# Kernel optimization log

Measured on AMD Instinct MI355X. Metric: run time of the kernel, lower is better.

The kernel has to match this reference:

```python
import jax, jax.numpy as jnp
import numpy as np

N_EMBD = 768
N_HEAD = 12
B, T = 2, 2048


def setup_inputs() -> dict:
    key = jax.random.key(0)
    ks = jax.random.split(key, 8)
    C = N_EMBD
    s = 0.02
    return {
        "x": jax.random.normal(ks[0], (B, T, C), jnp.float32),
        "ln1_g": jnp.ones((C,), jnp.float32),
        "ln1_b": jnp.zeros((C,), jnp.float32),
        "w_attn": jax.random.normal(ks[1], (C, 3 * C), jnp.float32) * s,
        "b_attn": jnp.zeros((3 * C,), jnp.float32),
        "w_attn_proj": jax.random.normal(ks[2], (C, C), jnp.float32) * s,
        "b_attn_proj": jnp.zeros((C,), jnp.float32),
        "ln2_g": jnp.ones((C,), jnp.float32),
        "ln2_b": jnp.zeros((C,), jnp.float32),
        "w_fc": jax.random.normal(ks[3], (C, 4 * C), jnp.float32) * s,
        "b_fc": jnp.zeros((4 * C,), jnp.float32),
        "w_mlp_proj": jax.random.normal(ks[4], (4 * C, C), jnp.float32) * s,
        "b_mlp_proj": jnp.zeros((C,), jnp.float32),
    }


def _layernorm(x, g, b, eps=1e-5):
    mu = jnp.mean(x, axis=-1, keepdims=True)
    var = jnp.mean(jnp.square(x - mu), axis=-1, keepdims=True)
    return (x - mu) * jax.lax.rsqrt(var + eps) * g + b


def _new_gelu(x):
    c = np.sqrt(2.0 / np.pi).astype(np.float32)
    return 0.5 * x * (1.0 + jnp.tanh(c * (x + 0.044715 * x * x * x)))


def _block(x, ln1_g, ln1_b, w_attn, b_attn, w_attn_proj, b_attn_proj,
           ln2_g, ln2_b, w_fc, b_fc, w_mlp_proj, b_mlp_proj):
    Bx, Tx, C = x.shape
    hd = C // N_HEAD
    h = _layernorm(x, ln1_g, ln1_b)
    qkv = h @ w_attn + b_attn  # [B,T,3C]
    q, k, v = jnp.split(qkv, 3, axis=-1)
    # [B,H,T,hd]
    q = q.reshape(Bx, Tx, N_HEAD, hd).transpose(0, 2, 1, 3)
    k = k.reshape(Bx, Tx, N_HEAD, hd).transpose(0, 2, 1, 3)
    v = v.reshape(Bx, Tx, N_HEAD, hd).transpose(0, 2, 1, 3)
    att = jnp.einsum('bhqd,bhkd->bhqk', q, k) * (1.0 / np.sqrt(hd))
    causal = jnp.tril(jnp.ones((Tx, Tx), bool))
    att = jnp.where(causal[None, None], att, -jnp.inf)
    att = jax.nn.softmax(att, axis=-1)
    y = jnp.einsum('bhqk,bhkd->bhqd', att, v)
    y = y.transpose(0, 2, 1, 3).reshape(Bx, Tx, C)
    x = x + y @ w_attn_proj + b_attn_proj
    h2 = _layernorm(x, ln2_g, ln2_b)
    x = x + _new_gelu(h2 @ w_fc + b_fc) @ w_mlp_proj + b_mlp_proj
    return x


def reference(x, ln1_g, ln1_b, w_attn, b_attn, w_attn_proj, b_attn_proj,
              ln2_g, ln2_b, w_fc, b_fc, w_mlp_proj, b_mlp_proj):
    return _block(x, ln1_g, ln1_b, w_attn, b_attn, w_attn_proj, b_attn_proj,
                  ln2_g, ln2_b, w_fc, b_fc, w_mlp_proj, b_mlp_proj)
```

## Files before the change

kernel.cpp:

```cpp
#include <hip/hip_runtime.h>
#include <hip/hip_bf16.h>
#include <math.h>

#define N_EMBD 768
#define N_HEAD 12
#define BATCH  2
#define SEQ    2048
#define ROWS   (BATCH*SEQ)
#define C3     (3*N_EMBD)

typedef __bf16 bf16;
typedef __attribute__((ext_vector_type(8))) __bf16 bf16x8;
typedef __attribute__((ext_vector_type(4))) float f32x4;

__device__ __forceinline__ void async16(const bf16* g, bf16* l) {
    __builtin_amdgcn_global_load_lds(
        (const __attribute__((address_space(1))) uint32_t*)g,
        (__attribute__((address_space(3))) uint32_t*)l, 16, 0, 0);
}

__global__ __launch_bounds__(256) void k_transpose_cast(
    const float* __restrict__ in, bf16* __restrict__ out, int K, int N)
{
    __shared__ bf16 tile[32][33];
    int n0 = blockIdx.x * 32, k0 = blockIdx.y * 32;
    int tc = threadIdx.x & 31, tr = threadIdx.x >> 5;
    #pragma unroll
    for (int i = 0; i < 4; i++) {
        int r = tr + i * 8;
        tile[r][tc] = (bf16)in[(size_t)(k0 + r) * N + n0 + tc];
    }
    __syncthreads();
    #pragma unroll
    for (int i = 0; i < 4; i++) {
        int r = tr + i * 8;
        out[(size_t)(n0 + r) * K + k0 + tc] = tile[tc][r];
    }
}

__global__ __launch_bounds__(256) void k_vtrans(
    const bf16* __restrict__ qkv, bf16* __restrict__ vt)
{
    __shared__ bf16 tile[32][33];
    int tt = blockIdx.x;
    int bh = blockIdx.y;
    int dt = blockIdx.z;
    int b = bh / N_HEAD, h = bh % N_HEAD;
    int tc = threadIdx.x & 31, tr = threadIdx.x >> 5;
    #pragma unroll
    for (int i = 0; i < 4; i++) {
        int r = tr + i * 8;
        tile[r][tc] = qkv[(size_t)(b * SEQ + tt * 32 + r) * C3 + 2 * N_EMBD + h * 64 + dt * 32 + tc];
    }
    __syncthreads();
    #pragma unroll
    for (int i = 0; i < 4; i++) {
        int r = tr + i * 8;
        vt[(size_t)(bh * 64 + dt * 32 + r) * SEQ + tt * 32 + tc] = tile[tc][r];
    }
}

__global__ __launch_bounds__(256) void k_layernorm(
    const float* __restrict__ x, const float* __restrict__ g,
    const float* __restrict__ b, bf16* __restrict__ out)
{
    int wave = threadIdx.x >> 6, lane = threadIdx.x & 63;
    int row = blockIdx.x * 4 + wave;
    const float* xr = x + (size_t)row * N_EMBD;
    float v[12];
    float s = 0.f, sq = 0.f;
    #pragma unroll
    for (int i = 0; i < 12; i++) {
        v[i] = xr[lane + 64 * i];
        s += v[i]; sq += v[i] * v[i];
    }
    #pragma unroll
    for (int off = 32; off > 0; off >>= 1) {
        s  += __shfl_xor(s, off);
        sq += __shfl_xor(sq, off);
    }
    float mu  = s * (1.f / N_EMBD);
    float var = sq * (1.f / N_EMBD) - mu * mu;
    float rs  = rsqrtf(var + 1e-5f);
    bf16* orow = out + (size_t)row * N_EMBD;
    #pragma unroll
    for (int i = 0; i < 12; i++) {
        int c = lane + 64 * i;
        orow[c] = (bf16)((v[i] - mu) * rs * g[c] + b[c]);
    }
}

template<int BN, int ACT, bool RES, bool OUT_BF16>
__global__ __launch_bounds__(256) void k_gemm(
    const bf16* __restrict__ A, const bf16* __restrict__ Bt,
    const float* __restrict__ bias, const float* __restrict__ res,
    void* __restrict__ outp, int M, int N, int K)
{
    constexpr int WC  = BN / 64;
    constexpr int WR  = 4 / WC;
    constexpr int RPW = 128 / WR;
    constexpr int MI  = RPW / 16;
    __shared__ __align__(16) bf16 As[128 * 64];
    __shared__ __align__(16) bf16 Bs[BN * 64];
    int n0 = blockIdx.x * BN, m0 = blockIdx.y * 128;
    int t = threadIdx.x;
    int lane = t & 63, wave = t >> 6;
    int wr = wave / WC, wc = wave % WC;
    int quad = lane >> 4, l16 = lane & 15;

    f32x4 acc[MI][4];
    #pragma unroll
    for (int i = 0; i < MI; i++)
        #pragma unroll
        for (int j = 0; j < 4; j++) acc[i][j] = (f32x4){0.f, 0.f, 0.f, 0.f};

    int sr = t >> 3;
    int sc = t & 7;
    int gsw = (sc ^ (sr & 7)) * 8;

    for (int k0 = 0; k0 < K; k0 += 64) {
        __syncthreads();
        #pragma unroll
        for (int p = 0; p < 4; p++) {
            int r = sr + p * 32;
            async16(&A[(size_t)(m0 + r) * K + k0 + gsw], &As[r * 64 + sc * 8]);
        }
        #pragma unroll
        for (int p = 0; p < BN / 32; p++) {
            int r = sr + p * 32;
            async16(&Bt[(size_t)(n0 + r) * K + k0 + gsw], &Bs[r * 64 + sc * 8]);
        }
        __syncthreads();
        #pragma unroll
        for (int kh = 0; kh < 2; kh++) {
            bf16x8 af[MI], bfv[4];
            #pragma unroll
            for (int i = 0; i < MI; i++)
                af[i]  = *(bf16x8*)&As[(wr * RPW + i * 16 + l16) * 64 + (((quad + 4 * kh) ^ (l16 & 7)) * 8)];
            #pragma unroll
            for (int j = 0; j < 4; j++)
                bfv[j] = *(bf16x8*)&Bs[(wc * 64 + j * 16 + l16) * 64 + (((quad + 4 * kh) ^ (l16 & 7)) * 8)];
            #pragma unroll
            for (int i = 0; i < MI; i++)
                #pragma unroll
                for (int j = 0; j < 4; j++)
                    acc[i][j] = __builtin_amdgcn_mfma_f32_16x16x32_bf16(af[i], bfv[j], acc[i][j], 0, 0, 0);
        }
    }

    float* outf = (float*)outp;
    bf16*  outb = (bf16*)outp;
    #pragma unroll
    for (int i = 0; i < MI; i++) {
        #pragma unroll
        for (int j = 0; j < 4; j++) {
            int col = n0 + wc * 64 + j * 16 + l16;
            float bv = bias[col];
            #pragma unroll
            for (int r = 0; r < 4; r++) {
                int row = m0 + wr * RPW + i * 16 + quad * 4 + r;
                float v = acc[i][j][r] + bv;
                if (ACT == 1) {
                    float z = 0.7978845608f * (v + 0.044715f * v * v * v);
                    v = v / (1.f + __expf(-2.f * z));
                }
                if (RES) v += res[(size_t)row * N + col];
                if (OUT_BF16) outb[(size_t)row * N + col] = (bf16)v;
                else          outf[(size_t)row * N + col] = v;
            }
        }
    }
}

#define PS_S 72
__global__ __launch_bounds__(256) void k_flash(
    const bf16* __restrict__ qkv, const bf16* __restrict__ vt, bf16* __restrict__ y)
{
    __shared__ __align__(16) bf16 Ks[64 * 64];
    __shared__ __align__(16) bf16 VTl[64 * 64];
    __shared__ __align__(16) bf16 Ps[4][16 * PS_S];
    int bid = blockIdx.x;
    int u = bid >> 1, sb = bid & 1;
    int v = u & 31, w = u >> 5;
    int bh = 2 * w + sb;
    int qt = sb ? 31 - v : v;
    int b = bh / N_HEAD, h = bh % N_HEAD;
    int t = threadIdx.x, lane = t & 63, wave = t >> 6;
    int quad = lane >> 4, l16 = lane & 15;
    int qbase = qt * 64 + wave * 16;

    bf16x8 qa[2];
    {
        const bf16* qrow = qkv + (size_t)(b * SEQ + qbase + l16) * C3 + h * 64;
        #pragma unroll
        for (int kh = 0; kh < 2; kh++) {
            union { uint4 u4; bf16 e[8]; bf16x8 vv; } uq;
            uq.u4 = *(const uint4*)&qrow[quad * 8 + kh * 32];
            #pragma unroll
            for (int j = 0; j < 8; j++) uq.e[j] = (bf16)((float)uq.e[j] * 0.125f);
            qa[kh] = uq.vv;
        }
    }
    float l_part[4] = {0.f, 0.f, 0.f, 0.f};
    f32x4 o[4];
    #pragma unroll
    for (int j = 0; j < 4; j++) o[j] = (f32x4){0.f, 0.f, 0.f, 0.f};

    int sr = t >> 3;
    int sc = t & 7;
    int gsw = (sc ^ (sr & 7)) * 8;

    for (int k0 = 0; k0 <= qt * 64; k0 += 64) {
        __syncthreads();
        #pragma unroll
        for (int p = 0; p < 2; p++) {
            int kr = sr + 32 * p;
            async16(&qkv[(size_t)(b * SEQ + k0 + kr) * C3 + N_EMBD + h * 64 + gsw],
                    &Ks[kr * 64 + sc * 8]);
        }
        #pragma unroll
        for (int p = 0; p < 2; p++) {
            int dr = sr + 32 * p;
            async16(&vt[(size_t)(bh * 64 + dr) * SEQ + k0 + gsw],
                    &VTl[dr * 64 + sc * 8]);
        }
        __syncthreads();

        f32x4 s[4];
        #pragma unroll
        for (int nt = 0; nt < 4; nt++) {
            bf16x8 b0 = *(bf16x8*)&Ks[(nt * 16 + l16) * 64 + (((quad    ) ^ (l16 & 7)) * 8)];
            bf16x8 b1 = *(bf16x8*)&Ks[(nt * 16 + l16) * 64 + (((quad + 4) ^ (l16 & 7)) * 8)];
            f32x4 z = (f32x4){0.f, 0.f, 0.f, 0.f};
            z = __builtin_amdgcn_mfma_f32_16x16x32_bf16(qa[0], b0, z, 0, 0, 0);
            z = __builtin_amdgcn_mfma_f32_16x16x32_bf16(qa[1], b1, z, 0, 0, 0);
            s[nt] = z;
        }
        bool diag = (k0 == qt * 64);
        float p[4][4];
        #pragma unroll
        for (int nt = 0; nt < 4; nt++) {
            int key = k0 + nt * 16 + l16;
            #pragma unroll
            for (int r = 0; r < 4; r++) {
                float pv = __expf(s[nt][r]);
                if (diag && key > qbase + quad * 4 + r) pv = 0.f;
                p[nt][r] = pv;
                l_part[r] += pv;
            }
        }
        #pragma unroll
        for (int nt = 0; nt < 4; nt++)
            #pragma unroll
            for (int r = 0; r < 4; r++)
                Ps[wave][(quad * 4 + r) * PS_S + nt * 16 + l16] = (bf16)p[nt][r];
        bf16x8 pa[2];
        #pragma unroll
        for (int kt = 0; kt < 2; kt++)
            pa[kt] = *(bf16x8*)&Ps[wave][l16 * PS_S + kt * 32 + quad * 8];
        #pragma unroll
        for (int jt = 0; jt < 4; jt++) {
            int d = jt * 16 + l16;
            #pragma unroll
            for (int kt = 0; kt < 2; kt++) {
                bf16x8 vb = *(bf16x8*)&VTl[d * 64 + (((quad + 4 * kt) ^ (l16 & 7)) * 8)];
                o[jt] = __builtin_amdgcn_mfma_f32_16x16x32_bf16(pa[kt], vb, o[jt], 0, 0, 0);
            }
        }
    }
    #pragma unroll
    for (int r = 0; r < 4; r++) {
        #pragma unroll
        for (int off = 8; off > 0; off >>= 1) l_part[r] += __shfl_xor(l_part[r], off);
    }
    #pragma unroll
    for (int jt = 0; jt < 4; jt++)
        #pragma unroll
        for (int r = 0; r < 4; r++) {
            int q = qbase + quad * 4 + r;
            y[(size_t)(b * SEQ + q) * N_EMBD + h * 64 + jt * 16 + l16] =
                (bf16)(o[jt][r] / l_part[r]);
        }
}

extern "C" void kernel_launch(void* const* d_in, const int* in_sizes, int n_in,
                              void* d_out, int out_size, void* d_ws, size_t ws_size,
                              hipStream_t stream) {
    const float* x           = (const float*)d_in[0];
    const float* ln1_g       = (const float*)d_in[1];
    const float* ln1_b       = (const float*)d_in[2];
    const float* w_attn      = (const float*)d_in[3];
    const float* b_attn      = (const float*)d_in[4];
    const float* w_attn_proj = (const float*)d_in[5];
    const float* b_attn_proj = (const float*)d_in[6];
    const float* ln2_g       = (const float*)d_in[7];
    const float* ln2_b       = (const float*)d_in[8];
    const float* w_fc        = (const float*)d_in[9];
    const float* b_fc        = (const float*)d_in[10];
    const float* w_mlp_proj  = (const float*)d_in[11];
    const float* b_mlp_proj  = (const float*)d_in[12];

    char* ws = (char*)d_ws;
    size_t off = 0;
    auto alloc = [&](size_t n) -> void* {
        off = (off + 255) & ~(size_t)255;
        void* p = ws + off;
        off += n;
        return p;
    };
    bf16* wqkvT  = (bf16*)alloc((size_t)C3 * N_EMBD * 2);
    bf16* wprojT = (bf16*)alloc((size_t)N_EMBD * N_EMBD * 2);
    bf16* wfcT   = (bf16*)alloc((size_t)4 * N_EMBD * N_EMBD * 2);
    bf16* wmlpT  = (bf16*)alloc((size_t)N_EMBD * 4 * N_EMBD * 2);
    bf16* hbuf   = (bf16*)alloc((size_t)ROWS * N_EMBD * 2);
    float* x2    = (float*)alloc((size_t)ROWS * N_EMBD * 4);
    bf16* yb     = (bf16*)alloc((size_t)ROWS * N_EMBD * 2);
    bf16* vtb    = (bf16*)alloc((size_t)BATCH * N_HEAD * 64 * SEQ * 2);
    bf16* big    = (bf16*)alloc((size_t)ROWS * 4 * N_EMBD * 2);
    bf16* qkvb   = big;
    bf16* actb   = big;

    k_transpose_cast<<<dim3(C3 / 32,     N_EMBD / 32), 256, 0, stream>>>(w_attn,      wqkvT,  N_EMBD, C3);
    k_transpose_cast<<<dim3(N_EMBD / 32, N_EMBD / 32), 256, 0, stream>>>(w_attn_proj, wprojT, N_EMBD, N_EMBD);
    k_transpose_cast<<<dim3(3072 / 32,   N_EMBD / 32), 256, 0, stream>>>(w_fc,        wfcT,   N_EMBD, 3072);
    k_transpose_cast<<<dim3(N_EMBD / 32, 3072 / 32),   256, 0, stream>>>(w_mlp_proj,  wmlpT,  3072,   N_EMBD);

    k_layernorm<<<ROWS / 4, 256, 0, stream>>>(x, ln1_g, ln1_b, hbuf);
    k_gemm<128, 0, false, true ><<<dim3(C3 / 128,  ROWS / 128), 256, 0, stream>>>(hbuf, wqkvT,  b_attn,      nullptr, qkvb, ROWS, C3,     N_EMBD);
    k_vtrans<<<dim3(SEQ / 32, BATCH * N_HEAD, 2), 256, 0, stream>>>(qkvb, vtb);
    k_flash<<<768, 256, 0, stream>>>(qkvb, vtb, yb);
    k_gemm<64,  0, true,  false><<<dim3(N_EMBD / 64, ROWS / 128), 256, 0, stream>>>(yb,   wprojT, b_attn_proj, x,       x2,   ROWS, N_EMBD, N_EMBD);
    k_layernorm<<<ROWS / 4, 256, 0, stream>>>(x2, ln2_g, ln2_b, hbuf);
    k_gemm<128, 1, false, true ><<<dim3(3072 / 128, ROWS / 128), 256, 0, stream>>>(hbuf, wfcT,   b_fc,        nullptr, actb, ROWS, 3072,   N_EMBD);
    k_gemm<64,  0, true,  false><<<dim3(N_EMBD / 64, ROWS / 128), 256, 0, stream>>>(actb, wmlpT,  b_mlp_proj,  x2, (float*)d_out, ROWS, N_EMBD, 3072);
}
```

Before: 297.8 us.

## Fuse V transpose into QKV GEMM, merge weight casts, double-buffer flash loads

```diff
diff --git a/kernel.cpp b/kernel.cpp
--- a/kernel.cpp
+++ b/kernel.cpp
@@ -19,11 +19,21 @@
         (__attribute__((address_space(3))) uint32_t*)l, 16, 0, 0);
 }
 
-__global__ __launch_bounds__(256) void k_transpose_cast(
-    const float* __restrict__ in, bf16* __restrict__ out, int K, int N)
+__global__ __launch_bounds__(256) void k_transpose_all(
+    const float* __restrict__ w0, bf16* __restrict__ o0,
+    const float* __restrict__ w1, bf16* __restrict__ o1,
+    const float* __restrict__ w2, bf16* __restrict__ o2,
+    const float* __restrict__ w3, bf16* __restrict__ o3)
 {
     __shared__ bf16 tile[32][33];
-    int n0 = blockIdx.x * 32, k0 = blockIdx.y * 32;
+    int bid = blockIdx.x;
+    const float* in; bf16* out; int K, N, local;
+    if      (bid < 1728) { in = w0; out = o0; K = 768;  N = 2304; local = bid; }
+    else if (bid < 2304) { in = w1; out = o1; K = 768;  N = 768;  local = bid - 1728; }
+    else if (bid < 4608) { in = w2; out = o2; K = 768;  N = 3072; local = bid - 2304; }
+    else                 { in = w3; out = o3; K = 3072; N = 768;  local = bid - 4608; }
+    int nt = N / 32;
+    int n0 = (local % nt) * 32, k0 = (local / nt) * 32;
     int tc = threadIdx.x & 31, tr = threadIdx.x >> 5;
     #pragma unroll
     for (int i = 0; i < 4; i++) {
@@ -35,28 +45,6 @@
     for (int i = 0; i < 4; i++) {
         int r = tr + i * 8;
         out[(size_t)(n0 + r) * K + k0 + tc] = tile[tc][r];
-    }
-}
-
-__global__ __launch_bounds__(256) void k_vtrans(
-    const bf16* __restrict__ qkv, bf16* __restrict__ vt)
-{
-    __shared__ bf16 tile[32][33];
-    int tt = blockIdx.x;
-    int bh = blockIdx.y;
-    int dt = blockIdx.z;
-    int b = bh / N_HEAD, h = bh % N_HEAD;
-    int tc = threadIdx.x & 31, tr = threadIdx.x >> 5;
-    #pragma unroll
-    for (int i = 0; i < 4; i++) {
-        int r = tr + i * 8;
-        tile[r][tc] = qkv[(size_t)(b * SEQ + tt * 32 + r) * C3 + 2 * N_EMBD + h * 64 + dt * 32 + tc];
-    }
-    __syncthreads();
-    #pragma unroll
-    for (int i = 0; i < 4; i++) {
-        int r = tr + i * 8;
-        vt[(size_t)(bh * 64 + dt * 32 + r) * SEQ + tt * 32 + tc] = tile[tc][r];
     }
 }
 
@@ -90,11 +78,11 @@
     }
 }
 
-template<int BN, int ACT, bool RES, bool OUT_BF16>
+template<int BN, int ACT, bool RES, bool OUT_BF16, bool VOUT>
 __global__ __launch_bounds__(256) void k_gemm(
     const bf16* __restrict__ A, const bf16* __restrict__ Bt,
     const float* __restrict__ bias, const float* __restrict__ res,
-    void* __restrict__ outp, int M, int N, int K)
+    void* __restrict__ outp, bf16* __restrict__ vout, int M, int N, int K)
 {
     constexpr int WC  = BN / 64;
     constexpr int WR  = 4 / WC;
@@ -148,6 +136,25 @@
         }
     }
 
+    if (VOUT && n0 >= 1536) {
+        #pragma unroll
+        for (int i = 0; i < MI; i++) {
+            #pragma unroll
+            for (int j = 0; j < 4; j++) {
+                int col = n0 + wc * 64 + j * 16 + l16;
+                int hv = (col - 1536) >> 6, dv = (col - 1536) & 63;
+                float bv = bias[col];
+                int row0 = m0 + wr * RPW + i * 16 + quad * 4;
+                int bb = row0 >> 11, ts = row0 & 2047;
+                union { ushort4 u4; bf16 e[4]; } pk;
+                #pragma unroll
+                for (int r = 0; r < 4; r++) pk.e[r] = (bf16)(acc[i][j][r] + bv);
+                *(ushort4*)&vout[((size_t)(bb * N_HEAD + hv) * 64 + dv) * SEQ + ts] = pk.u4;
+            }
+        }
+        return;
+    }
+
     float* outf = (float*)outp;
     bf16*  outb = (bf16*)outp;
     #pragma unroll
@@ -176,8 +183,8 @@
 __global__ __launch_bounds__(256) void k_flash(
     const bf16* __restrict__ qkv, const bf16* __restrict__ vt, bf16* __restrict__ y)
 {
-    __shared__ __align__(16) bf16 Ks[64 * 64];
-    __shared__ __align__(16) bf16 VTl[64 * 64];
+    __shared__ __align__(16) bf16 Ks[2][64 * 64];
+    __shared__ __align__(16) bf16 VTl[2][64 * 64];
     __shared__ __align__(16) bf16 Ps[4][16 * PS_S];
     int bid = blockIdx.x;
     int u = bid >> 1, sb = bid & 1;
@@ -210,33 +217,39 @@
     int sc = t & 7;
     int gsw = (sc ^ (sr & 7)) * 8;
 
-    for (int k0 = 0; k0 <= qt * 64; k0 += 64) {
+    const bf16* kg = qkv + (size_t)b * SEQ * C3 + N_EMBD + h * 64;
+    const bf16* vg = vt + (size_t)bh * 64 * SEQ;
+
+    auto stage = [&](int tile, int bufi) {
+        int k0 = tile * 64;
+        #pragma unroll
+        for (int p = 0; p < 2; p++) {
+            int rr = sr + 32 * p;
+            async16(&kg[(size_t)(k0 + rr) * C3 + gsw],  &Ks[bufi][rr * 64 + sc * 8]);
+            async16(&vg[(size_t)rr * SEQ + k0 + gsw], &VTl[bufi][rr * 64 + sc * 8]);
+        }
+    };
+
+    int ntiles = qt + 1;
+    stage(0, 0);
+
+    for (int tt = 0; tt < ntiles; tt++) {
+        int bufi = tt & 1;
+        int k0 = tt * 64;
         __syncthreads();
-        #pragma unroll
-        for (int p = 0; p < 2; p++) {
-            int kr = sr + 32 * p;
-            async16(&qkv[(size_t)(b * SEQ + k0 + kr) * C3 + N_EMBD + h * 64 + gsw],
-                    &Ks[kr * 64 + sc * 8]);
-        }
-        #pragma unroll
-        for (int p = 0; p < 2; p++) {
-            int dr = sr + 32 * p;
-            async16(&vt[(size_t)(bh * 64 + dr) * SEQ + k0 + gsw],
-                    &VTl[dr * 64 + sc * 8]);
-        }
-        __syncthreads();
+        if (tt + 1 < ntiles) stage(tt + 1, bufi ^ 1);
 
         f32x4 s[4];
         #pragma unroll
         for (int nt = 0; nt < 4; nt++) {
-            bf16x8 b0 = *(bf16x8*)&Ks[(nt * 16 + l16) * 64 + (((quad    ) ^ (l16 & 7)) * 8)];
-            bf16x8 b1 = *(bf16x8*)&Ks[(nt * 16 + l16) * 64 + (((quad + 4) ^ (l16 & 7)) * 8)];
+            bf16x8 b0 = *(bf16x8*)&Ks[bufi][(nt * 16 + l16) * 64 + (((quad    ) ^ (l16 & 7)) * 8)];
+            bf16x8 b1 = *(bf16x8*)&Ks[bufi][(nt * 16 + l16) * 64 + (((quad + 4) ^ (l16 & 7)) * 8)];
             f32x4 z = (f32x4){0.f, 0.f, 0.f, 0.f};
             z = __builtin_amdgcn_mfma_f32_16x16x32_bf16(qa[0], b0, z, 0, 0, 0);
             z = __builtin_amdgcn_mfma_f32_16x16x32_bf16(qa[1], b1, z, 0, 0, 0);
             s[nt] = z;
         }
-        bool diag = (k0 == qt * 64);
+        bool diag = (tt == qt);
         float p[4][4];
         #pragma unroll
         for (int nt = 0; nt < 4; nt++) {
@@ -263,7 +276,7 @@
             int d = jt * 16 + l16;
             #pragma unroll
             for (int kt = 0; kt < 2; kt++) {
-                bf16x8 vb = *(bf16x8*)&VTl[d * 64 + (((quad + 4 * kt) ^ (l16 & 7)) * 8)];
+                bf16x8 vb = *(bf16x8*)&VTl[bufi][d * 64 + (((quad + 4 * kt) ^ (l16 & 7)) * 8)];
                 o[jt] = __builtin_amdgcn_mfma_f32_16x16x32_bf16(pa[kt], vb, o[jt], 0, 0, 0);
             }
         }
@@ -320,17 +333,18 @@
     bf16* qkvb   = big;
     bf16* actb   = big;
 
-    k_transpose_cast<<<dim3(C3 / 32,     N_EMBD / 32), 256, 0, stream>>>(w_attn,      wqkvT,  N_EMBD, C3);
-    k_transpose_cast<<<dim3(N_EMBD / 32, N_EMBD / 32), 256, 0, stream>>>(w_attn_proj, wprojT, N_EMBD, N_EMBD);
-    k_transpose_cast<<<dim3(3072 / 32,   N_EMBD / 32), 256, 0, stream>>>(w_fc,        wfcT,   N_EMBD, 3072);
-    k_transpose_cast<<<dim3(N_EMBD / 32, 3072 / 32),   256, 0, stream>>>(w_mlp_proj,  wmlpT,  3072,   N_EMBD);
+    k_transpose_all<<<6912, 256, 0, stream>>>(w_attn, wqkvT, w_attn_proj, wprojT,
+                                              w_fc, wfcT, w_mlp_proj, wmlpT);
 
     k_layernorm<<<ROWS / 4, 256, 0, stream>>>(x, ln1_g, ln1_b, hbuf);
-    k_gemm<128, 0, false, true ><<<dim3(C3 / 128,  ROWS / 128), 256, 0, stream>>>(hbuf, wqkvT,  b_attn,      nullptr, qkvb, ROWS, C3,     N_EMBD);
-    k_vtrans<<<dim3(SEQ / 32, BATCH * N_HEAD, 2), 256, 0, stream>>>(qkvb, vtb);
+    k_gemm<128, 0, false, true,  true ><<<dim3(C3 / 128,  ROWS / 128), 256, 0, stream>>>(
+        hbuf, wqkvT,  b_attn,      nullptr, qkvb, vtb,     ROWS, C3,     N_EMBD);
     k_flash<<<768, 256, 0, stream>>>(qkvb, vtb, yb);
-    k_gemm<64,  0, true,  false><<<dim3(N_EMBD / 64, ROWS / 128), 256, 0, stream>>>(yb,   wprojT, b_attn_proj, x,       x2,   ROWS, N_EMBD, N_EMBD);
+    k_gemm<64,  0, true,  false, false><<<dim3(N_EMBD / 64, ROWS / 128), 256, 0, stream>>>(
+        yb,   wprojT, b_attn_proj, x,       x2,   nullptr, ROWS, N_EMBD, N_EMBD);
     k_layernorm<<<ROWS / 4, 256, 0, stream>>>(x2, ln2_g, ln2_b, hbuf);
-    k_gemm<128, 1, false, true ><<<dim3(3072 / 128, ROWS / 128), 256, 0, stream>>>(hbuf, wfcT,   b_fc,        nullptr, actb, ROWS, 3072,   N_EMBD);
-    k_gemm<64,  0, true,  false><<<dim3(N_EMBD / 64, ROWS / 128), 256, 0, stream>>>(actb, wmlpT,  b_mlp_proj,  x2, (float*)d_out, ROWS, N_EMBD, 3072);
-}
+    k_gemm<128, 1, false, true,  false><<<dim3(3072 / 128, ROWS / 128), 256, 0, stream>>>(
+        hbuf, wfcT,   b_fc,        nullptr, actb, nullptr, ROWS, 3072,   N_EMBD);
+    k_gemm<64,  0, true,  false, false><<<dim3(N_EMBD / 64, ROWS / 128), 256, 0, stream>>>(
+        actb, wmlpT,  b_mlp_proj,  x2, (float*)d_out, nullptr, ROWS, N_EMBD, 3072);
+}
```

Result: slower. 304.0 us (+2.1%).
